# Kernel tuning notes

Measured on AMD Instinct MI355X. Metric: run time of the kernel, lower is better.

The kernel has to match this reference:

```python
import jax, jax.numpy as jnp
import numpy as np

B, N, IN_DIM = 8, 1024, 64
HID, OUT = 96, 128
NEG_SLOPE = 0.2
LN_EPS = 1e-5


def setup_inputs() -> dict:
    key = jax.random.key(0)
    ks = iter(jax.random.split(key, 32))
    d = {}
    d['x'] = jax.random.normal(next(ks), (B, N, IN_DIM), dtype=jnp.float32)
    d['adj'] = jax.random.randint(next(ks), (N, N), 0, 2, dtype=jnp.int32)
    # pre: LayerNorm + Linear(in->hid)
    d['ln_g'] = jnp.ones((IN_DIM,), jnp.float32)
    d['ln_b'] = jnp.zeros((IN_DIM,), jnp.float32)
    d['pre_w'] = jax.random.normal(next(ks), (IN_DIM, HID)) * 0.05
    d['pre_b'] = jnp.zeros((HID,), jnp.float32)
    # gat1: 3 heads of dim 32, concat; gat2-5: 1 head of dim 96, mean
    def gat_params(h, dim):
        w = jax.random.normal(next(ks), (HID, h * dim)) * 0.05
        a_s = jax.random.normal(next(ks), (h, dim)) * 0.05
        a_d = jax.random.normal(next(ks), (h, dim)) * 0.05
        return w, a_s, a_d
    d['g1_w'], d['g1_as'], d['g1_ad'] = gat_params(3, HID // 3)
    d['g2_w'], d['g2_as'], d['g2_ad'] = gat_params(1, HID)
    d['g3_w'], d['g3_as'], d['g3_ad'] = gat_params(1, HID)
    d['g4_w'], d['g4_as'], d['g4_ad'] = gat_params(1, HID)
    d['g5_w'], d['g5_as'], d['g5_ad'] = gat_params(1, HID)
    # sym_gate: Linear(2*hid -> hid//2), ELU, Linear(hid//2 -> 2), Sigmoid
    d['gate_w1'] = jax.random.normal(next(ks), (2 * HID, HID // 2)) * 0.05
    d['gate_b1'] = jnp.zeros((HID // 2,), jnp.float32)
    d['gate_w2'] = jax.random.normal(next(ks), (HID // 2, 2)) * 0.05
    d['gate_b2'] = jnp.zeros((2,), jnp.float32)
    # embed_proj: Linear(3*hid -> out)
    d['proj_w'] = jax.random.normal(next(ks), (3 * HID, OUT)) * 0.05
    d['proj_b'] = jnp.zeros((OUT,), jnp.float32)
    return d


def _gat(x, adj_mask, W, a_src, a_dst, concat):
    b, n, _ = x.shape
    h_heads, dim = a_src.shape
    h = (x @ W).reshape(b, n, h_heads, dim).transpose(0, 2, 1, 3)  # [B,H,N,D]
    e_src = jnp.einsum('bhnd,hd->bhn', h, a_src)
    e_dst = jnp.einsum('bhnd,hd->bhn', h, a_dst)
    # e[b,h,i,j] = leaky_relu(e_src[i] + e_dst[j])
    e = jax.nn.leaky_relu(e_src[..., :, None] + e_dst[..., None, :], NEG_SLOPE)
    e = jnp.where(adj_mask[None, None, :, :], e, jnp.float32(-1e9))
    attn = jax.nn.softmax(e, axis=-1)  # dropout is identity in eval mode
    out = jnp.einsum('bhij,bhjd->bhid', attn, h)
    if concat:
        return out.transpose(0, 2, 1, 3).reshape(b, n, h_heads * dim)
    return out.mean(axis=1)


def reference(x, adj, ln_g, ln_b, pre_w, pre_b,
              g1_w, g1_as, g1_ad, g2_w, g2_as, g2_ad,
              g3_w, g3_as, g3_ad, g4_w, g4_as, g4_ad,
              g5_w, g5_as, g5_ad,
              gate_w1, gate_b1, gate_w2, gate_b2, proj_w, proj_b):
    mask = adj > 0  # [N,N] bool
    # pre: LayerNorm -> Linear -> ELU (dropout = identity, eval mode)
    mu = x.mean(-1, keepdims=True)
    var = ((x - mu) ** 2).mean(-1, keepdims=True)
    xn = (x - mu) * jax.lax.rsqrt(var + LN_EPS) * ln_g + ln_b
    x0 = jax.nn.elu(xn @ pre_w + pre_b)
    x1 = jax.nn.elu(_gat(x0, mask, g1_w, g1_as, g1_ad, concat=True))
    x2 = jax.nn.elu(_gat(x1, mask, g2_w, g2_as, g2_ad, concat=False))
    pooled = jnp.concatenate([x1.mean(axis=1), x2.mean(axis=1)], axis=-1)  # [B,2*hid]
    gates = jax.nn.sigmoid(jax.nn.elu(pooled @ gate_w1 + gate_b1) @ gate_w2 + gate_b2)  # [B,2]
    w_t = gates[:, 0][:, None, None]
    w_r = gates[:, 1][:, None, None]
    td_in = (1.0 - w_t) * x1 + w_t * x2
    ra_in = (1.0 - w_r) * x1 + w_r * x2
    x4 = jax.nn.elu(_gat(td_in, mask, g4_w, g4_as, g4_ad, concat=False))
    x5 = jax.nn.elu(_gat(ra_in, mask, g5_w, g5_as, g5_ad, concat=False))
    stage_in = x2 + 0.5 * (w_t * x4 + w_r * x5)
    x3 = jax.nn.elu(_gat(stage_in, mask, g3_w, g3_as, g3_ad, concat=False))
    graph_token = jnp.concatenate([x3.mean(axis=1), x4.mean(axis=1), x5.mean(axis=1)], axis=-1)
    embed = jax.nn.elu(graph_token @ proj_w + proj_b)
    return (embed, gates[:, 0], gates[:, 1])
```

## Files before the change

### kernel.cpp

```cpp
#include <hip/hip_runtime.h>
#include <math.h>

#define Bq 8
#define Nn 1024
#define IND 64
#define HIDD 96

typedef __attribute__((ext_vector_type(8))) short bf16x8_t;
typedef __attribute__((ext_vector_type(4))) float f32x4_t;
typedef unsigned int u32;

__device__ __forceinline__ float elu_f(float x){ return x > 0.f ? x : __expf(x) - 1.f; }
__device__ __forceinline__ float lrelu_f(float x){ return x > 0.f ? x : 0.2f * x; }
__device__ __forceinline__ short f2bf(float f){
    union { float f; u32 u; } v; v.f = f;
    u32 r = (v.u + 0x7FFFu + ((v.u >> 16) & 1u)) >> 16;
    return (short)r;
}

__global__ __launch_bounds__(256) void pack_adj(const int* __restrict__ adj, u32* __restrict__ adjp)
{
    int w = blockIdx.x * 256 + threadIdx.x;
    int row = w >> 5, wc = w & 31;
    const int* p = adj + (size_t)row * Nn + wc * 32;
    u32 b = 0;
    #pragma unroll
    for (int e = 0; e < 32; e++) b |= (p[e] > 0 ? 1u : 0u) << e;
    adjp[w] = b;
}

struct PrepArgs { const float *W, *as_, *ad_; int H; };
struct Prep5 { PrepArgs a[5]; };

__global__ __launch_bounds__(96) void prep_w(Prep5 p, short* __restrict__ Wt)
{
    const int c = blockIdx.x, g = blockIdx.y, k = threadIdx.x;
    const PrepArgs A = p.a[g];
    float v = 0.f;
    if (c < 96) v = A.W[k * 96 + c];
    else {
        int q = c - 96, dim = 96 / A.H;
        if (q < A.H) { if (k >= q * dim && k < (q + 1) * dim) v = A.as_[k]; }
        else if (q < 2 * A.H) { int hh = q - A.H; if (k >= hh * dim && k < (hh + 1) * dim) v = A.ad_[k]; }
    }
    Wt[((size_t)g * 112 + c) * 96 + k] = f2bf(v);
}

__global__ __launch_bounds__(256) void pre_kernel(
    const float* __restrict__ x, const float* __restrict__ ln_g, const float* __restrict__ ln_b,
    const float* __restrict__ w, const float* __restrict__ bias, float* __restrict__ x0)
{
    __shared__ float xs[32][68];
    __shared__ float wl[IND * HIDD];
    __shared__ float gl[IND], bl[IND];
    __shared__ float mu[32], rv[32];
    const int t = threadIdx.x;
    const int i0 = blockIdx.x * 32, b = blockIdx.y;

    {
        const float4* w4 = (const float4*)w;
        float4* wl4 = (float4*)wl;
        #pragma unroll
        for (int m = 0; m < 6; m++) wl4[t + 256 * m] = w4[t + 256 * m];
    }
    if (t < IND) { gl[t] = ln_g[t]; bl[t] = ln_b[t]; }
    {
        const float4* xg = (const float4*)(x + ((size_t)b * Nn + i0) * IND);
        #pragma unroll
        for (int m = 0; m < 2; m++) {
            int idx = t + 256 * m;
            int r = idx >> 4, c4 = idx & 15;
            float4 v = xg[idx];
            xs[r][c4 * 4 + 0] = v.x; xs[r][c4 * 4 + 1] = v.y;
            xs[r][c4 * 4 + 2] = v.z; xs[r][c4 * 4 + 3] = v.w;
        }
    }
    __syncthreads();
    const int r = t >> 3, cg = t & 7;
    {
        float s = 0.f, s2 = 0.f;
        #pragma unroll
        for (int k = 0; k < 8; k++) { float v = xs[r][cg * 8 + k]; s += v; s2 += v * v; }
        #pragma unroll
        for (int m = 1; m < 8; m <<= 1) { s += __shfl_xor(s, m); s2 += __shfl_xor(s2, m); }
        if (cg == 0) {
            float mean = s * (1.f / IND);
            mu[r] = mean;
            rv[r] = rsqrtf(s2 * (1.f / IND) - mean * mean + 1e-5f);
        }
    }
    __syncthreads();
    float acc[12];
    #pragma unroll
    for (int c = 0; c < 12; c++) acc[c] = 0.f;
    const float mur = mu[r], rvr = rv[r];
    for (int k = 0; k < IND; k++) {
        float xn = (xs[r][k] - mur) * rvr * gl[k] + bl[k];
        const float4* wrow = (const float4*)(&wl[k * HIDD + cg * 12]);
        #pragma unroll
        for (int q = 0; q < 3; q++) {
            float4 wv = wrow[q];
            acc[q * 4 + 0] += xn * wv.x; acc[q * 4 + 1] += xn * wv.y;
            acc[q * 4 + 2] += xn * wv.z; acc[q * 4 + 3] += xn * wv.w;
        }
    }
    #pragma unroll
    for (int c = 0; c < 12; c++) acc[c] = elu_f(acc[c] + bias[cg * 12 + c]);
    float4* o4 = (float4*)(x0 + ((size_t)b * Nn + i0 + r) * HIDD + cg * 12);
    o4[0] = make_float4(acc[0], acc[1], acc[2], acc[3]);
    o4[1] = make_float4(acc[4], acc[5], acc[6], acc[7]);
    o4[2] = make_float4(acc[8], acc[9], acc[10], acc[11]);
}

struct HArgs {
    const float *xa, *xb, *xc;
    const short* Wt;
    float *es, *ed;
    short *ht;
    int mode, H;
};

__global__ __launch_bounds__(256) void h_mfma(HArgs a0, HArgs a1, const float* __restrict__ gates)
{
    const int t = threadIdx.x;
    const int lane = t & 63, w = t >> 6;
    const int node0 = blockIdx.x * 16;
    const int b = node0 >> 10, n0 = node0 & 1023;
    const HArgs A = blockIdx.y ? a1 : a0;
    const int row16 = lane & 15, grp = lane >> 4;

    float wt = 0.f, wr = 0.f;
    if (A.mode == 1) wt = gates[b * 2 + 0];
    else if (A.mode == 2) wt = gates[b * 2 + 1];
    else if (A.mode == 3) { wt = gates[b * 2 + 0]; wr = gates[b * 2 + 1]; }

    const size_t rowoff = (size_t)(node0 + row16) * HIDD;
    const int nt0 = (w < 3) ? 2 * w : 6;

    f32x4_t acc0 = {0.f,0.f,0.f,0.f}, acc1 = {0.f,0.f,0.f,0.f};
    #pragma unroll
    for (int ks = 0; ks < 3; ks++) {
        const int k0 = ks * 32 + grp * 8;
        float xv[8];
        {
            const float* pa = A.xa + rowoff + k0;
            float4 v0 = *(const float4*)pa, v1 = *(const float4*)(pa + 4);
            xv[0]=v0.x; xv[1]=v0.y; xv[2]=v0.z; xv[3]=v0.w;
            xv[4]=v1.x; xv[5]=v1.y; xv[6]=v1.z; xv[7]=v1.w;
        }
        if (A.mode == 1 || A.mode == 2) {
            const float* pb = A.xb + rowoff + k0;
            float4 u0 = *(const float4*)pb, u1 = *(const float4*)(pb + 4);
            float yv[8] = {u0.x,u0.y,u0.z,u0.w,u1.x,u1.y,u1.z,u1.w};
            #pragma unroll
            for (int e = 0; e < 8; e++) xv[e] = (1.f - wt) * xv[e] + wt * yv[e];
        } else if (A.mode == 3) {
            const float* pb = A.xb + rowoff + k0;
            const float* pc = A.xc + rowoff + k0;
            float4 u0 = *(const float4*)pb, u1 = *(const float4*)(pb + 4);
            float4 q0 = *(const float4*)pc, q1 = *(const float4*)(pc + 4);
            float yv[8] = {u0.x,u0.y,u0.z,u0.w,u1.x,u1.y,u1.z,u1.w};
            float zv[8] = {q0.x,q0.y,q0.z,q0.w,q1.x,q1.y,q1.z,q1.w};
            #pragma unroll
            for (int e = 0; e < 8; e++) xv[e] = xv[e] + 0.5f * (wt * yv[e] + wr * zv[e]);
        }
        bf16x8_t af;
        #pragma unroll
        for (int e = 0; e < 8; e++) af[e] = f2bf(xv[e]);

        {
            const short* wp0 = A.Wt + (size_t)(nt0 * 16 + row16) * 96 + k0;
            bf16x8_t bf0 = *(const bf16x8_t*)wp0;
            acc0 = __builtin_amdgcn_mfma_f32_16x16x32_bf16(af, bf0, acc0, 0, 0, 0);
        }
        if (w < 3) {
            const short* wp1 = A.Wt + (size_t)((nt0 + 1) * 16 + row16) * 96 + k0;
            bf16x8_t bf1 = *(const bf16x8_t*)wp1;
            acc1 = __builtin_amdgcn_mfma_f32_16x16x32_bf16(af, bf1, acc1, 0, 0, 0);
        }
    }
    if (w < 3) {
        u32 lo0 = ((u32)(unsigned short)f2bf(acc0[0])) | (((u32)(unsigned short)f2bf(acc0[1])) << 16);
        u32 hi0 = ((u32)(unsigned short)f2bf(acc0[2])) | (((u32)(unsigned short)f2bf(acc0[3])) << 16);
        int c0 = nt0 * 16 + row16;
        *(uint2*)(A.ht + ((size_t)b * 96 + c0) * Nn + n0 + grp * 4) = make_uint2(lo0, hi0);
        u32 lo1 = ((u32)(unsigned short)f2bf(acc1[0])) | (((u32)(unsigned short)f2bf(acc1[1])) << 16);
        u32 hi1 = ((u32)(unsigned short)f2bf(acc1[2])) | (((u32)(unsigned short)f2bf(acc1[3])) << 16);
        int c1 = c0 + 16;
        *(uint2*)(A.ht + ((size_t)b * 96 + c1) * Nn + n0 + grp * 4) = make_uint2(lo1, hi1);
    } else {
        int q = row16;
        if (q < 2 * A.H) {
            int head = (q < A.H) ? q : q - A.H;
            float* dst = ((q < A.H) ? A.es : A.ed) + ((size_t)b * A.H + head) * Nn + n0 + grp * 4;
            *(float4*)dst = make_float4(acc0[0], acc0[1], acc0[2], acc0[3]);
        }
    }
}

struct WArgs {
    const short* ht;
    const float* es;
    const float* ed;
    float* out;
    float* msum;
};

template<int DIM, int NH, bool DUAL>
__global__ __launch_bounds__(256) void ws_kernel(const u32* __restrict__ adjp, WArgs a0, WArgs a1)
{
    constexpr int NT = DIM / 16;
    __shared__ u32 adjl[16][33];
    __shared__ float esl[16];
    __shared__ float red[4][16][DIM + 1];
    __shared__ float redz[4][16];
    __shared__ float colsum[DIM];
    const int t = threadIdx.x;
    const int i0 = blockIdx.x * 16;
    const int by = blockIdx.y, b = blockIdx.z;
    const WArgs A = (DUAL && by) ? a1 : a0;
    const int h_in = DUAL ? 0 : by;
    const int colbase = h_in * DIM;

    if (t < 128) {
        int r = t >> 3, w4 = (t & 7) * 4;
        uint4 wv = *(const uint4*)(adjp + (size_t)(i0 + r) * 32 + w4);
        adjl[r][w4] = wv.x; adjl[r][w4 + 1] = wv.y; adjl[r][w4 + 2] = wv.z; adjl[r][w4 + 3] = wv.w;
    }
    if (t < 16) esl[t] = A.es[((size_t)b * NH + h_in) * Nn + i0 + t];
    if (t < DIM) colsum[t] = 0.f;
    __syncthreads();

    const int lane = t & 63, w = t >> 6;
    const int row16 = lane & 15, grp = lane >> 4;
    const int jb = w * 256;
    const float es_r = esl[row16];
    const float* edp = A.ed + ((size_t)b * NH + h_in) * Nn + jb + grp * 8;
    const short* hrow = A.ht + ((size_t)b * 96 + colbase + row16) * Nn + jb + grp * 8;

    f32x4_t acc[NT];
    #pragma unroll
    for (int n = 0; n < NT; n++) acc[n] = (f32x4_t){0.f, 0.f, 0.f, 0.f};
    f32x4_t accz = {0.f, 0.f, 0.f, 0.f};
    bf16x8_t ones;
    #pragma unroll
    for (int e = 0; e < 8; e++) ones[e] = (short)0x3F80;

    #pragma unroll
    for (int ks = 0; ks < 8; ks++) {
        u32 bits = adjl[row16][w * 8 + ks] >> (grp * 8);
        float4 e0 = *(const float4*)(edp + ks * 32);
        float4 e1 = *(const float4*)(edp + ks * 32 + 4);
        float ev[8] = {e0.x, e0.y, e0.z, e0.w, e1.x, e1.y, e1.z, e1.w};
        bf16x8_t af;
        #pragma unroll
        for (int e = 0; e < 8; e++) {
            float p = __expf(lrelu_f(es_r + ev[e]));
            af[e] = f2bf(((bits >> e) & 1) ? p : 0.f);
        }
        #pragma unroll
        for (int n = 0; n < NT; n++) {
            bf16x8_t bf = *(const bf16x8_t*)(hrow + n * 16 * Nn + ks * 32);
            acc[n] = __builtin_amdgcn_mfma_f32_16x16x32_bf16(af, bf, acc[n], 0, 0, 0);
        }
        accz = __builtin_amdgcn_mfma_f32_16x16x32_bf16(af, ones, accz, 0, 0, 0);
    }

    #pragma unroll
    for (int n = 0; n < NT; n++)
        #pragma unroll
        for (int reg = 0; reg < 4; reg++)
            red[w][grp * 4 + reg][n * 16 + row16] = acc[n][reg];
    if (row16 == 0) {
        #pragma unroll
        for (int reg = 0; reg < 4; reg++) redz[w][grp * 4 + reg] = accz[reg];
    }
    __syncthreads();

    #pragma unroll
    for (int q = 0; q < (16 * DIM) / 256; q++) {
        int idx = t + q * 256;
        int r = idx / DIM, c = idx % DIM;
        float s = red[0][r][c] + red[1][r][c] + red[2][r][c] + red[3][r][c];
        float z = redz[0][r] + redz[1][r] + redz[2][r] + redz[3][r];
        float o = elu_f(s / z);
        A.out[((size_t)b * Nn + i0 + r) * HIDD + colbase + c] = o;
        atomicAdd(&colsum[c], o);
    }
    __syncthreads();
    if (t < DIM) atomicAdd(&A.msum[b * HIDD + colbase + t], colsum[t]);
}

__global__ __launch_bounds__(64) void gates_kernel(
    const float* __restrict__ x1s, const float* __restrict__ x2s,
    const float* __restrict__ w1, const float* __restrict__ b1,
    const float* __restrict__ w2, const float* __restrict__ b2,
    float* __restrict__ gates, float* __restrict__ d_out)
{
    __shared__ float pl[192], hid[48];
    const int b = blockIdx.x, t = threadIdx.x;
    for (int k = t; k < 192; k += 64)
        pl[k] = ((k < HIDD) ? x1s[b * HIDD + k] : x2s[b * HIDD + k - HIDD]) * (1.f / Nn);
    __syncthreads();
    if (t < 48) {
        float acc = b1[t];
        for (int k = 0; k < 192; k++) acc += pl[k] * w1[k * 48 + t];
        hid[t] = elu_f(acc);
    }
    __syncthreads();
    if (t < 2) {
        float acc = b2[t];
        for (int k = 0; k < 48; k++) acc += hid[k] * w2[k * 2 + t];
        float g = 1.f / (1.f + __expf(-acc));
        gates[b * 2 + t] = g;
        d_out[1024 + t * 8 + b] = g;
    }
}

__global__ __launch_bounds__(128) void proj_kernel(
    const float* __restrict__ x3s, const float* __restrict__ x4s, const float* __restrict__ x5s,
    const float* __restrict__ w, const float* __restrict__ bias, float* __restrict__ d_out)
{
    __shared__ float tok[288];
    const int b = blockIdx.x, t = threadIdx.x;
    if (t < HIDD) {
        tok[t]            = x3s[b * HIDD + t] * (1.f / Nn);
        tok[HIDD + t]     = x4s[b * HIDD + t] * (1.f / Nn);
        tok[2 * HIDD + t] = x5s[b * HIDD + t] * (1.f / Nn);
    }
    __syncthreads();
    float acc = bias[t];
    for (int k = 0; k < 288; k++) acc += tok[k] * w[k * 128 + t];
    d_out[b * 128 + t] = elu_f(acc);
}

extern "C" void kernel_launch(void* const* d_in, const int* in_sizes, int n_in,
                              void* d_out, int out_size, void* d_ws, size_t ws_size,
                              hipStream_t stream)
{
    const float* x     = (const float*)d_in[0];
    const int*   adj   = (const int*)d_in[1];
    const float* ln_g  = (const float*)d_in[2];
    const float* ln_b  = (const float*)d_in[3];
    const float* pre_w = (const float*)d_in[4];
    const float* pre_b = (const float*)d_in[5];
    const float* g_w[5]  = {(const float*)d_in[6],  (const float*)d_in[9],  (const float*)d_in[12],
                            (const float*)d_in[15], (const float*)d_in[18]};
    const float* g_as[5] = {(const float*)d_in[7],  (const float*)d_in[10], (const float*)d_in[13],
                            (const float*)d_in[16], (const float*)d_in[19]};
    const float* g_ad[5] = {(const float*)d_in[8],  (const float*)d_in[11], (const float*)d_in[14],
                            (const float*)d_in[17], (const float*)d_in[20]};
    const float* gw1 = (const float*)d_in[21];
    const float* gb1 = (const float*)d_in[22];
    const float* gw2 = (const float*)d_in[23];
    const float* gb2 = (const float*)d_in[24];
    const float* pw  = (const float*)d_in[25];
    const float* pb  = (const float*)d_in[26];
    float* out = (float*)d_out;

    float* ws = (float*)d_ws;
    const size_t SZ = (size_t)Bq * Nn * HIDD;
    float* x0 = ws;
    float* x1 = ws + 1 * SZ;
    float* x2 = ws + 2 * SZ;
    float* x3 = ws + 3 * SZ;
    float* x4 = ws + 4 * SZ;
    float* x5 = ws + 5 * SZ;
    float* esb = ws + 6 * SZ;
    float* edb = esb + 24576;
    short* ht0 = (short*)(edb + 24576);
    short* ht1 = ht0 + (size_t)Bq * 96 * Nn;
    short* wtb = ht1 + (size_t)Bq * 96 * Nn;
    float* msb = (float*)(wtb + 5 * 112 * 96);
    float* ms1 = msb, *ms2 = msb + 768, *ms3 = msb + 1536, *ms4 = msb + 2304, *ms5 = msb + 3072;
    float* gts = msb + 3840;
    u32*   adjp = (u32*)(gts + 16);

    const dim3 blk256(256);

    hipMemsetAsync(msb, 0, 3840 * sizeof(float), stream);
    {
        Prep5 P;
        for (int g = 0; g < 5; g++) { P.a[g].W = g_w[g]; P.a[g].as_ = g_as[g]; P.a[g].ad_ = g_ad[g]; P.a[g].H = (g == 0) ? 3 : 1; }
        prep_w<<<dim3(112, 5), dim3(96), 0, stream>>>(P, wtb);
    }
    pack_adj<<<dim3(128), blk256, 0, stream>>>(adj, adjp);
    pre_kernel<<<dim3(Nn / 32, Bq), blk256, 0, stream>>>(x, ln_g, ln_b, pre_w, pre_b, x0);

    const dim3 hgrid1(Bq * Nn / 16, 1), hgrid2(Bq * Nn / 16, 2);

    {
        HArgs A; A.xa = x0; A.xb = nullptr; A.xc = nullptr;
        A.Wt = wtb + 0 * 112 * 96; A.es = esb; A.ed = edb; A.ht = ht0; A.mode = 0; A.H = 3;
        h_mfma<<<hgrid1, blk256, 0, stream>>>(A, A, gts);
        WArgs W0; W0.ht = ht0; W0.es = esb; W0.ed = edb; W0.out = x1; W0.msum = ms1;
        ws_kernel<32, 3, false><<<dim3(Nn / 16, 3, Bq), blk256, 0, stream>>>(adjp, W0, W0);
    }
    {
        HArgs A; A.xa = x1; A.xb = nullptr; A.xc = nullptr;
        A.Wt = wtb + 1 * 112 * 96; A.es = esb; A.ed = edb; A.ht = ht0; A.mode = 0; A.H = 1;
        h_mfma<<<hgrid1, blk256, 0, stream>>>(A, A, gts);
        WArgs W0; W0.ht = ht0; W0.es = esb; W0.ed = edb; W0.out = x2; W0.msum = ms2;
        ws_kernel<96, 1, false><<<dim3(Nn / 16, 1, Bq), blk256, 0, stream>>>(adjp, W0, W0);
    }
    gates_kernel<<<dim3(Bq), dim3(64), 0, stream>>>(ms1, ms2, gw1, gb1, gw2, gb2, gts, out);

    {
        HArgs A0; A0.xa = x1; A0.xb = x2; A0.xc = nullptr;
        A0.Wt = wtb + 3 * 112 * 96; A0.es = esb; A0.ed = edb; A0.ht = ht0; A0.mode = 1; A0.H = 1;
        HArgs A1; A1.xa = x1; A1.xb = x2; A1.xc = nullptr;
        A1.Wt = wtb + 4 * 112 * 96; A1.es = esb + 8192; A1.ed = edb + 8192; A1.ht = ht1; A1.mode = 2; A1.H = 1;
        h_mfma<<<hgrid2, blk256, 0, stream>>>(A0, A1, gts);
        WArgs W0; W0.ht = ht0; W0.es = esb; W0.ed = edb; W0.out = x4; W0.msum = ms4;
        WArgs W1; W1.ht = ht1; W1.es = esb + 8192; W1.ed = edb + 8192; W1.out = x5; W1.msum = ms5;
        ws_kernel<96, 1, true><<<dim3(Nn / 16, 2, Bq), blk256, 0, stream>>>(adjp, W0, W1);
    }
    {
        HArgs A; A.xa = x2; A.xb = x4; A.xc = x5;
        A.Wt = wtb + 2 * 112 * 96; A.es = esb; A.ed = edb; A.ht = ht0; A.mode = 3; A.H = 1;
        h_mfma<<<hgrid1, blk256, 0, stream>>>(A, A, gts);
        WArgs W0; W0.ht = ht0; W0.es = esb; W0.ed = edb; W0.out = x3; W0.msum = ms3;
        ws_kernel<96, 1, false><<<dim3(Nn / 16, 1, Bq), blk256, 0, stream>>>(adjp, W0, W0);
    }

    proj_kernel<<<dim3(Bq), dim3(128), 0, stream>>>(ms3, ms4, ms5, pw, pb, out);
}
```

Measured before the change: 260.2 us.

## Fuse projections into aggregation kernels using linearity of gated inputs

```diff
diff --git a/kernel.cpp b/kernel.cpp
--- a/kernel.cpp
+++ b/kernel.cpp
@@ -3,8 +3,6 @@
 
 #define Bq 8
 #define Nn 1024
-#define IND 64
-#define HIDD 96
 
 typedef __attribute__((ext_vector_type(8))) short bf16x8_t;
 typedef __attribute__((ext_vector_type(4))) float f32x4_t;
@@ -14,306 +12,333 @@
 __device__ __forceinline__ float lrelu_f(float x){ return x > 0.f ? x : 0.2f * x; }
 __device__ __forceinline__ short f2bf(float f){
     union { float f; u32 u; } v; v.f = f;
-    u32 r = (v.u + 0x7FFFu + ((v.u >> 16) & 1u)) >> 16;
-    return (short)r;
-}
-
-__global__ __launch_bounds__(256) void pack_adj(const int* __restrict__ adj, u32* __restrict__ adjp)
-{
-    int w = blockIdx.x * 256 + threadIdx.x;
-    int row = w >> 5, wc = w & 31;
-    const int* p = adj + (size_t)row * Nn + wc * 32;
-    u32 b = 0;
+    return (short)((v.u + 0x7FFFu + ((v.u >> 16) & 1u)) >> 16);
+}
+__device__ __forceinline__ u32 pk2(float a, float b){
+    return (u32)(unsigned short)f2bf(a) | ((u32)(unsigned short)f2bf(b) << 16);
+}
+__device__ __forceinline__ bf16x8_t cvt8(const float* p){
+    bf16x8_t r;
     #pragma unroll
-    for (int e = 0; e < 32; e++) b |= (p[e] > 0 ? 1u : 0u) << e;
-    adjp[w] = b;
-}
-
-struct PrepArgs { const float *W, *as_, *ad_; int H; };
-struct Prep5 { PrepArgs a[5]; };
-
-__global__ __launch_bounds__(96) void prep_w(Prep5 p, short* __restrict__ Wt)
-{
-    const int c = blockIdx.x, g = blockIdx.y, k = threadIdx.x;
-    const PrepArgs A = p.a[g];
-    float v = 0.f;
-    if (c < 96) v = A.W[k * 96 + c];
-    else {
-        int q = c - 96, dim = 96 / A.H;
-        if (q < A.H) { if (k >= q * dim && k < (q + 1) * dim) v = A.as_[k]; }
-        else if (q < 2 * A.H) { int hh = q - A.H; if (k >= hh * dim && k < (hh + 1) * dim) v = A.ad_[k]; }
-    }
-    Wt[((size_t)g * 112 + c) * 96 + k] = f2bf(v);
-}
-
-__global__ __launch_bounds__(256) void pre_kernel(
+    for (int e = 0; e < 8; e++) r[e] = f2bf(p[e]);
+    return r;
+}
+
+struct PrepP {
+    const float *W0,*W1,*W2,*W3,*W4;
+    const float *s0,*s1,*s2,*s3,*s4;
+    const float *d0,*d1,*d2,*d3,*d4;
+};
+
+__global__ __launch_bounds__(256) void setup_kernel(
+    PrepP P, const int* __restrict__ adj, const float* __restrict__ pre_w,
+    u32* __restrict__ adjp, short* __restrict__ wtb, short* __restrict__ wpre,
+    float* __restrict__ msz)
+{
+    const int bid = blockIdx.x, t = threadIdx.x;
+    if (bid < 128) {
+        int w = bid * 256 + t;
+        int row = w >> 5, wc = w & 31;
+        const int* p = adj + (size_t)row * Nn + wc * 32;
+        u32 bset = 0;
+        #pragma unroll
+        for (int e = 0; e < 32; e++) bset |= (p[e] > 0 ? 1u : 0u) << e;
+        adjp[w] = bset;
+    } else if (bid < 338) {
+        int idx = (bid - 128) * 256 + t;
+        int g = idx / 10752, rem = idx % 10752;
+        int c = rem / 96, k = rem % 96;
+        const float* W  = (g==0)?P.W0:(g==1)?P.W1:(g==2)?P.W2:(g==3)?P.W3:P.W4;
+        const float* as = (g==0)?P.s0:(g==1)?P.s1:(g==2)?P.s2:(g==3)?P.s3:P.s4;
+        const float* ad = (g==0)?P.d0:(g==1)?P.d1:(g==2)?P.d2:(g==3)?P.d3:P.d4;
+        const int H = (g == 0) ? 3 : 1, dim = 96 / H;
+        float v = 0.f;
+        if (c < 96) v = W[k * 96 + c];
+        else {
+            int q = c - 96;
+            if (q < H) {
+                int base = q * dim; float s = 0.f;
+                for (int d = 0; d < dim; d++) s += W[k * 96 + base + d] * as[base + d];
+                v = s;
+            } else if (q < 2 * H) {
+                int base = (q - H) * dim; float s = 0.f;
+                for (int d = 0; d < dim; d++) s += W[k * 96 + base + d] * ad[base + d];
+                v = s;
+            }
+        }
+        wtb[idx] = f2bf(v);
+    } else if (bid < 362) {
+        int idx = (bid - 338) * 256 + t;
+        int c = idx >> 6, k = idx & 63;
+        wpre[idx] = f2bf(pre_w[k * 96 + c]);
+    } else {
+        int idx = (bid - 362) * 256 + t;
+        if (idx < 3856) msz[idx] = 0.f;
+    }
+}
+
+__global__ __launch_bounds__(256) void pre_h1(
     const float* __restrict__ x, const float* __restrict__ ln_g, const float* __restrict__ ln_b,
-    const float* __restrict__ w, const float* __restrict__ bias, float* __restrict__ x0)
-{
-    __shared__ float xs[32][68];
-    __shared__ float wl[IND * HIDD];
-    __shared__ float gl[IND], bl[IND];
-    __shared__ float mu[32], rv[32];
+    const short* __restrict__ wpre, const float* __restrict__ pre_b,
+    const short* __restrict__ Wt1, short* __restrict__ ht1,
+    float* __restrict__ es1, float* __restrict__ ed1)
+{
+    __shared__ short xsA[16][72];
+    __shared__ float xs0[16][100];
     const int t = threadIdx.x;
-    const int i0 = blockIdx.x * 32, b = blockIdx.y;
-
-    {
-        const float4* w4 = (const float4*)w;
-        float4* wl4 = (float4*)wl;
-        #pragma unroll
-        for (int m = 0; m < 6; m++) wl4[t + 256 * m] = w4[t + 256 * m];
-    }
-    if (t < IND) { gl[t] = ln_g[t]; bl[t] = ln_b[t]; }
-    {
-        const float4* xg = (const float4*)(x + ((size_t)b * Nn + i0) * IND);
-        #pragma unroll
-        for (int m = 0; m < 2; m++) {
-            int idx = t + 256 * m;
-            int r = idx >> 4, c4 = idx & 15;
-            float4 v = xg[idx];
-            xs[r][c4 * 4 + 0] = v.x; xs[r][c4 * 4 + 1] = v.y;
-            xs[r][c4 * 4 + 2] = v.z; xs[r][c4 * 4 + 3] = v.w;
-        }
-    }
-    __syncthreads();
-    const int r = t >> 3, cg = t & 7;
-    {
-        float s = 0.f, s2 = 0.f;
-        #pragma unroll
-        for (int k = 0; k < 8; k++) { float v = xs[r][cg * 8 + k]; s += v; s2 += v * v; }
-        #pragma unroll
-        for (int m = 1; m < 8; m <<= 1) { s += __shfl_xor(s, m); s2 += __shfl_xor(s2, m); }
-        if (cg == 0) {
-            float mean = s * (1.f / IND);
-            mu[r] = mean;
-            rv[r] = rsqrtf(s2 * (1.f / IND) - mean * mean + 1e-5f);
-        }
-    }
-    __syncthreads();
-    float acc[12];
-    #pragma unroll
-    for (int c = 0; c < 12; c++) acc[c] = 0.f;
-    const float mur = mu[r], rvr = rv[r];
-    for (int k = 0; k < IND; k++) {
-        float xn = (xs[r][k] - mur) * rvr * gl[k] + bl[k];
-        const float4* wrow = (const float4*)(&wl[k * HIDD + cg * 12]);
-        #pragma unroll
-        for (int q = 0; q < 3; q++) {
-            float4 wv = wrow[q];
-            acc[q * 4 + 0] += xn * wv.x; acc[q * 4 + 1] += xn * wv.y;
-            acc[q * 4 + 2] += xn * wv.z; acc[q * 4 + 3] += xn * wv.w;
-        }
-    }
-    #pragma unroll
-    for (int c = 0; c < 12; c++) acc[c] = elu_f(acc[c] + bias[cg * 12 + c]);
-    float4* o4 = (float4*)(x0 + ((size_t)b * Nn + i0 + r) * HIDD + cg * 12);
-    o4[0] = make_float4(acc[0], acc[1], acc[2], acc[3]);
-    o4[1] = make_float4(acc[4], acc[5], acc[6], acc[7]);
-    o4[2] = make_float4(acc[8], acc[9], acc[10], acc[11]);
-}
-
-struct HArgs {
-    const float *xa, *xb, *xc;
-    const short* Wt;
-    float *es, *ed;
-    short *ht;
-    int mode, H;
+    const int bid = blockIdx.x;
+    const int b = bid >> 6, n0 = (bid & 63) * 16;
+    {
+        int r = t >> 4, c4 = t & 15;
+        float4 v = *(const float4*)(x + ((size_t)b * Nn + n0 + r) * 64 + c4 * 4);
+        float s = v.x + v.y + v.z + v.w;
+        float s2 = v.x*v.x + v.y*v.y + v.z*v.z + v.w*v.w;
+        #pragma unroll
+        for (int m = 1; m < 16; m <<= 1) { s += __shfl_xor(s, m); s2 += __shfl_xor(s2, m); }
+        float mu = s * (1.f / 64), rv = rsqrtf(s2 * (1.f / 64) - mu * mu + 1e-5f);
+        float4 g = *(const float4*)(ln_g + c4 * 4);
+        float4 bb = *(const float4*)(ln_b + c4 * 4);
+        float xn0 = (v.x - mu) * rv * g.x + bb.x;
+        float xn1 = (v.y - mu) * rv * g.y + bb.y;
+        float xn2 = (v.z - mu) * rv * g.z + bb.z;
+        float xn3 = (v.w - mu) * rv * g.w + bb.w;
+        *(uint2*)&xsA[r][c4 * 4] = make_uint2(pk2(xn0, xn1), pk2(xn2, xn3));
+    }
+    __syncthreads();
+    const int lane = t & 63, w = t >> 6;
+    const int row16 = lane & 15, grp = lane >> 4;
+    for (int tile = w; tile < 6; tile += 4) {
+        f32x4_t acc = {0.f,0.f,0.f,0.f};
+        #pragma unroll
+        for (int ks = 0; ks < 2; ks++) {
+            int k0 = ks * 32 + grp * 8;
+            bf16x8_t af = *(const bf16x8_t*)&xsA[row16][k0];
+            bf16x8_t bf = *(const bf16x8_t*)(wpre + (size_t)(tile * 16 + row16) * 64 + k0);
+            acc = __builtin_amdgcn_mfma_f32_16x16x32_bf16(af, bf, acc, 0, 0, 0);
+        }
+        int col = tile * 16 + row16;
+        float pbv = pre_b[col];
+        #pragma unroll
+        for (int reg = 0; reg < 4; reg++)
+            xs0[grp * 4 + reg][col] = elu_f(acc[reg] + pbv);
+    }
+    __syncthreads();
+    for (int tile = w; tile < 7; tile += 4) {
+        f32x4_t acc = {0.f,0.f,0.f,0.f};
+        #pragma unroll
+        for (int ks = 0; ks < 3; ks++) {
+            int k0 = ks * 32 + grp * 8;
+            bf16x8_t af = cvt8(&xs0[row16][k0]);
+            bf16x8_t bf = *(const bf16x8_t*)(Wt1 + (size_t)(tile * 16 + row16) * 96 + k0);
+            acc = __builtin_amdgcn_mfma_f32_16x16x32_bf16(af, bf, acc, 0, 0, 0);
+        }
+        int col = tile * 16 + row16;
+        if (tile < 6) {
+            *(uint2*)(ht1 + ((size_t)b * 96 + col) * Nn + n0 + grp * 4) =
+                make_uint2(pk2(acc[0], acc[1]), pk2(acc[2], acc[3]));
+        } else {
+            int q = row16;
+            if (q < 3)
+                *(float4*)(es1 + ((size_t)b * 3 + q) * Nn + n0 + grp * 4) =
+                    make_float4(acc[0], acc[1], acc[2], acc[3]);
+            else if (q < 6)
+                *(float4*)(ed1 + ((size_t)b * 3 + (q - 3)) * Nn + n0 + grp * 4) =
+                    make_float4(acc[0], acc[1], acc[2], acc[3]);
+        }
+    }
+}
+
+struct WSArgs {
+    const float *es, *ed;
+    const short *ht;
+    float *ms;
+    int nmat, mode0;
+    const short *W0, *W1, *W2;
+    float *T0, *T1, *T2;
+    short *oHt; float *oEs, *oEd;
 };
 
-__global__ __launch_bounds__(256) void h_mfma(HArgs a0, HArgs a1, const float* __restrict__ gates)
-{
+template<int NH>
+__global__ __launch_bounds__(256) void ws_fused(const u32* __restrict__ adjp, WSArgs a0, WSArgs a1)
+{
+    constexpr int DIMH = 96 / NH, NT = DIMH / 16;
+    __shared__ float xrows[16][100];
+    __shared__ float red[4][16][97];
+    __shared__ float redz[4][16];
+    __shared__ u32 adjl[16][33];
+    __shared__ float esl[NH * 16];
     const int t = threadIdx.x;
-    const int lane = t & 63, w = t >> 6;
-    const int node0 = blockIdx.x * 16;
-    const int b = node0 >> 10, n0 = node0 & 1023;
-    const HArgs A = blockIdx.y ? a1 : a0;
-    const int row16 = lane & 15, grp = lane >> 4;
-
-    float wt = 0.f, wr = 0.f;
-    if (A.mode == 1) wt = gates[b * 2 + 0];
-    else if (A.mode == 2) wt = gates[b * 2 + 1];
-    else if (A.mode == 3) { wt = gates[b * 2 + 0]; wr = gates[b * 2 + 1]; }
-
-    const size_t rowoff = (size_t)(node0 + row16) * HIDD;
-    const int nt0 = (w < 3) ? 2 * w : 6;
-
-    f32x4_t acc0 = {0.f,0.f,0.f,0.f}, acc1 = {0.f,0.f,0.f,0.f};
-    #pragma unroll
-    for (int ks = 0; ks < 3; ks++) {
-        const int k0 = ks * 32 + grp * 8;
-        float xv[8];
-        {
-            const float* pa = A.xa + rowoff + k0;
-            float4 v0 = *(const float4*)pa, v1 = *(const float4*)(pa + 4);
-            xv[0]=v0.x; xv[1]=v0.y; xv[2]=v0.z; xv[3]=v0.w;
-            xv[4]=v1.x; xv[5]=v1.y; xv[6]=v1.z; xv[7]=v1.w;
-        }
-        if (A.mode == 1 || A.mode == 2) {
-            const float* pb = A.xb + rowoff + k0;
-            float4 u0 = *(const float4*)pb, u1 = *(const float4*)(pb + 4);
-            float yv[8] = {u0.x,u0.y,u0.z,u0.w,u1.x,u1.y,u1.z,u1.w};
-            #pragma unroll
-            for (int e = 0; e < 8; e++) xv[e] = (1.f - wt) * xv[e] + wt * yv[e];
-        } else if (A.mode == 3) {
-            const float* pb = A.xb + rowoff + k0;
-            const float* pc = A.xc + rowoff + k0;
-            float4 u0 = *(const float4*)pb, u1 = *(const float4*)(pb + 4);
-            float4 q0 = *(const float4*)pc, q1 = *(const float4*)(pc + 4);
-            float yv[8] = {u0.x,u0.y,u0.z,u0.w,u1.x,u1.y,u1.z,u1.w};
-            float zv[8] = {q0.x,q0.y,q0.z,q0.w,q1.x,q1.y,q1.z,q1.w};
-            #pragma unroll
-            for (int e = 0; e < 8; e++) xv[e] = xv[e] + 0.5f * (wt * yv[e] + wr * zv[e]);
-        }
-        bf16x8_t af;
-        #pragma unroll
-        for (int e = 0; e < 8; e++) af[e] = f2bf(xv[e]);
-
-        {
-            const short* wp0 = A.Wt + (size_t)(nt0 * 16 + row16) * 96 + k0;
-            bf16x8_t bf0 = *(const bf16x8_t*)wp0;
-            acc0 = __builtin_amdgcn_mfma_f32_16x16x32_bf16(af, bf0, acc0, 0, 0, 0);
-        }
-        if (w < 3) {
-            const short* wp1 = A.Wt + (size_t)((nt0 + 1) * 16 + row16) * 96 + k0;
-            bf16x8_t bf1 = *(const bf16x8_t*)wp1;
-            acc1 = __builtin_amdgcn_mfma_f32_16x16x32_bf16(af, bf1, acc1, 0, 0, 0);
-        }
-    }
-    if (w < 3) {
-        u32 lo0 = ((u32)(unsigned short)f2bf(acc0[0])) | (((u32)(unsigned short)f2bf(acc0[1])) << 16);
-        u32 hi0 = ((u32)(unsigned short)f2bf(acc0[2])) | (((u32)(unsigned short)f2bf(acc0[3])) << 16);
-        int c0 = nt0 * 16 + row16;
-        *(uint2*)(A.ht + ((size_t)b * 96 + c0) * Nn + n0 + grp * 4) = make_uint2(lo0, hi0);
-        u32 lo1 = ((u32)(unsigned short)f2bf(acc1[0])) | (((u32)(unsigned short)f2bf(acc1[1])) << 16);
-        u32 hi1 = ((u32)(unsigned short)f2bf(acc1[2])) | (((u32)(unsigned short)f2bf(acc1[3])) << 16);
-        int c1 = c0 + 16;
-        *(uint2*)(A.ht + ((size_t)b * 96 + c1) * Nn + n0 + grp * 4) = make_uint2(lo1, hi1);
-    } else {
-        int q = row16;
-        if (q < 2 * A.H) {
-            int head = (q < A.H) ? q : q - A.H;
-            float* dst = ((q < A.H) ? A.es : A.ed) + ((size_t)b * A.H + head) * Nn + n0 + grp * 4;
-            *(float4*)dst = make_float4(acc0[0], acc0[1], acc0[2], acc0[3]);
-        }
-    }
-}
-
-struct WArgs {
-    const short* ht;
-    const float* es;
-    const float* ed;
-    float* out;
-    float* msum;
-};
-
-template<int DIM, int NH, bool DUAL>
-__global__ __launch_bounds__(256) void ws_kernel(const u32* __restrict__ adjp, WArgs a0, WArgs a1)
-{
-    constexpr int NT = DIM / 16;
-    __shared__ u32 adjl[16][33];
-    __shared__ float esl[16];
-    __shared__ float red[4][16][DIM + 1];
-    __shared__ float redz[4][16];
-    __shared__ float colsum[DIM];
-    const int t = threadIdx.x;
-    const int i0 = blockIdx.x * 16;
-    const int by = blockIdx.y, b = blockIdx.z;
-    const WArgs A = (DUAL && by) ? a1 : a0;
-    const int h_in = DUAL ? 0 : by;
-    const int colbase = h_in * DIM;
+    const int i0 = blockIdx.x * 16, b = blockIdx.z;
+    const WSArgs A = blockIdx.y ? a1 : a0;
 
     if (t < 128) {
         int r = t >> 3, w4 = (t & 7) * 4;
         uint4 wv = *(const uint4*)(adjp + (size_t)(i0 + r) * 32 + w4);
-        adjl[r][w4] = wv.x; adjl[r][w4 + 1] = wv.y; adjl[r][w4 + 2] = wv.z; adjl[r][w4 + 3] = wv.w;
-    }
-    if (t < 16) esl[t] = A.es[((size_t)b * NH + h_in) * Nn + i0 + t];
-    if (t < DIM) colsum[t] = 0.f;
+        adjl[r][w4] = wv.x; adjl[r][w4+1] = wv.y; adjl[r][w4+2] = wv.z; adjl[r][w4+3] = wv.w;
+    }
+    if (t < NH * 16)
+        esl[t] = A.es[((size_t)b * NH + (t >> 4)) * Nn + i0 + (t & 15)];
     __syncthreads();
 
     const int lane = t & 63, w = t >> 6;
     const int row16 = lane & 15, grp = lane >> 4;
     const int jb = w * 256;
-    const float es_r = esl[row16];
-    const float* edp = A.ed + ((size_t)b * NH + h_in) * Nn + jb + grp * 8;
-    const short* hrow = A.ht + ((size_t)b * 96 + colbase + row16) * Nn + jb + grp * 8;
-
-    f32x4_t acc[NT];
-    #pragma unroll
-    for (int n = 0; n < NT; n++) acc[n] = (f32x4_t){0.f, 0.f, 0.f, 0.f};
-    f32x4_t accz = {0.f, 0.f, 0.f, 0.f};
     bf16x8_t ones;
     #pragma unroll
     for (int e = 0; e < 8; e++) ones[e] = (short)0x3F80;
 
     #pragma unroll
-    for (int ks = 0; ks < 8; ks++) {
-        u32 bits = adjl[row16][w * 8 + ks] >> (grp * 8);
-        float4 e0 = *(const float4*)(edp + ks * 32);
-        float4 e1 = *(const float4*)(edp + ks * 32 + 4);
-        float ev[8] = {e0.x, e0.y, e0.z, e0.w, e1.x, e1.y, e1.z, e1.w};
-        bf16x8_t af;
-        #pragma unroll
-        for (int e = 0; e < 8; e++) {
-            float p = __expf(lrelu_f(es_r + ev[e]));
-            af[e] = f2bf(((bits >> e) & 1) ? p : 0.f);
+    for (int h = 0; h < NH; h++) {
+        const float es_r = esl[h * 16 + row16];
+        const float* edp = A.ed + ((size_t)b * NH + h) * Nn + jb + grp * 8;
+        const short* hb_ = A.ht + ((size_t)b * 96 + h * DIMH) * Nn + jb + grp * 8;
+        f32x4_t acc[NT];
+        f32x4_t accz = {0.f,0.f,0.f,0.f};
+        #pragma unroll
+        for (int n = 0; n < NT; n++) acc[n] = (f32x4_t){0.f,0.f,0.f,0.f};
+        #pragma unroll
+        for (int ks = 0; ks < 8; ks++) {
+            u32 bits = adjl[row16][w * 8 + ks] >> (grp * 8);
+            float4 e0 = *(const float4*)(edp + ks * 32);
+            float4 e1 = *(const float4*)(edp + ks * 32 + 4);
+            float ev[8] = {e0.x,e0.y,e0.z,e0.w,e1.x,e1.y,e1.z,e1.w};
+            bf16x8_t af;
+            #pragma unroll
+            for (int e = 0; e < 8; e++) {
+                float p = __expf(lrelu_f(es_r + ev[e]));
+                af[e] = f2bf(((bits >> e) & 1) ? p : 0.f);
+            }
+            #pragma unroll
+            for (int n = 0; n < NT; n++) {
+                bf16x8_t bf = *(const bf16x8_t*)(hb_ + (size_t)(n * 16 + row16) * Nn + ks * 32);
+                acc[n] = __builtin_amdgcn_mfma_f32_16x16x32_bf16(af, bf, acc[n], 0, 0, 0);
+            }
+            accz = __builtin_amdgcn_mfma_f32_16x16x32_bf16(af, ones, accz, 0, 0, 0);
         }
         #pragma unroll
         for (int n = 0; n < NT; n++) {
-            bf16x8_t bf = *(const bf16x8_t*)(hrow + n * 16 * Nn + ks * 32);
-            acc[n] = __builtin_amdgcn_mfma_f32_16x16x32_bf16(af, bf, acc[n], 0, 0, 0);
-        }
-        accz = __builtin_amdgcn_mfma_f32_16x16x32_bf16(af, ones, accz, 0, 0, 0);
-    }
-
-    #pragma unroll
-    for (int n = 0; n < NT; n++)
-        #pragma unroll
-        for (int reg = 0; reg < 4; reg++)
-            red[w][grp * 4 + reg][n * 16 + row16] = acc[n][reg];
-    if (row16 == 0) {
-        #pragma unroll
-        for (int reg = 0; reg < 4; reg++) redz[w][grp * 4 + reg] = accz[reg];
-    }
-    __syncthreads();
-
-    #pragma unroll
-    for (int q = 0; q < (16 * DIM) / 256; q++) {
-        int idx = t + q * 256;
-        int r = idx / DIM, c = idx % DIM;
-        float s = red[0][r][c] + red[1][r][c] + red[2][r][c] + red[3][r][c];
-        float z = redz[0][r] + redz[1][r] + redz[2][r] + redz[3][r];
-        float o = elu_f(s / z);
-        A.out[((size_t)b * Nn + i0 + r) * HIDD + colbase + c] = o;
-        atomicAdd(&colsum[c], o);
-    }
-    __syncthreads();
-    if (t < DIM) atomicAdd(&A.msum[b * HIDD + colbase + t], colsum[t]);
-}
-
-__global__ __launch_bounds__(64) void gates_kernel(
-    const float* __restrict__ x1s, const float* __restrict__ x2s,
-    const float* __restrict__ w1, const float* __restrict__ b1,
-    const float* __restrict__ w2, const float* __restrict__ b2,
-    float* __restrict__ gates, float* __restrict__ d_out)
-{
-    __shared__ float pl[192], hid[48];
-    const int b = blockIdx.x, t = threadIdx.x;
-    for (int k = t; k < 192; k += 64)
-        pl[k] = ((k < HIDD) ? x1s[b * HIDD + k] : x2s[b * HIDD + k - HIDD]) * (1.f / Nn);
+            #pragma unroll
+            for (int reg = 0; reg < 4; reg++)
+                red[w][grp * 4 + reg][n * 16 + row16] = acc[n][reg];
+        }
+        if (row16 == 0) {
+            #pragma unroll
+            for (int reg = 0; reg < 4; reg++) redz[w][grp * 4 + reg] = accz[reg];
+        }
+        __syncthreads();
+        #pragma unroll
+        for (int idx = t; idx < 16 * DIMH; idx += 256) {
+            int r = idx / DIMH, c = idx % DIMH;
+            float s = red[0][r][c] + red[1][r][c] + red[2][r][c] + red[3][r][c];
+            float z = redz[0][r] + redz[1][r] + redz[2][r] + redz[3][r];
+            xrows[r][h * DIMH + c] = elu_f(s / z);
+        }
+        __syncthreads();
+    }
+
+    if (t < 96) {
+        float s = 0.f;
+        #pragma unroll
+        for (int r = 0; r < 16; r++) s += xrows[r][t];
+        atomicAdd(A.ms + b * 96 + t, s);
+    }
+
+    for (int job = w; job < A.nmat * 7; job += 4) {
+        int mat = job / 7, tile = job - mat * 7;
+        const short* Wm = (mat == 0) ? A.W0 : (mat == 1) ? A.W1 : A.W2;
+        f32x4_t acc = {0.f,0.f,0.f,0.f};
+        #pragma unroll
+        for (int ks = 0; ks < 3; ks++) {
+            int k0 = ks * 32 + grp * 8;
+            bf16x8_t af = cvt8(&xrows[row16][k0]);
+            bf16x8_t bf = *(const bf16x8_t*)(Wm + (size_t)(tile * 16 + row16) * 96 + k0);
+            acc = __builtin_amdgcn_mfma_f32_16x16x32_bf16(af, bf, acc, 0, 0, 0);
+        }
+        int col = tile * 16 + row16;
+        if (mat == 0 && A.mode0 == 2) {
+            if (tile < 6) {
+                *(uint2*)(A.oHt + ((size_t)b * 96 + col) * Nn + i0 + grp * 4) =
+                    make_uint2(pk2(acc[0], acc[1]), pk2(acc[2], acc[3]));
+            } else if (row16 == 0) {
+                *(float4*)(A.oEs + (size_t)b * Nn + i0 + grp * 4) = make_float4(acc[0],acc[1],acc[2],acc[3]);
+            } else if (row16 == 1) {
+                *(float4*)(A.oEd + (size_t)b * Nn + i0 + grp * 4) = make_float4(acc[0],acc[1],acc[2],acc[3]);
+            }
+        } else {
+            float* Td = (mat == 0) ? A.T0 : (mat == 1) ? A.T1 : A.T2;
+            *(float4*)(Td + ((size_t)b * 112 + col) * Nn + i0 + grp * 4) =
+                make_float4(acc[0], acc[1], acc[2], acc[3]);
+        }
+    }
+}
+
+__global__ __launch_bounds__(256) void gates_combine(
+    const float* __restrict__ ms1, const float* __restrict__ ms2,
+    const float* __restrict__ gw1, const float* __restrict__ gb1,
+    const float* __restrict__ gw2, const float* __restrict__ gb2,
+    const float* __restrict__ U4, const float* __restrict__ V4,
+    const float* __restrict__ U5, const float* __restrict__ V5,
+    short* __restrict__ ht4, float* __restrict__ es4, float* __restrict__ ed4,
+    short* __restrict__ ht5, float* __restrict__ es5, float* __restrict__ ed5,
+    float* __restrict__ gts, float* __restrict__ d_out)
+{
+    __shared__ float pl[192], hid[48], gsh[2];
+    const int t = threadIdx.x, b = blockIdx.z, y = blockIdx.y, rr = blockIdx.x;
+    if (t < 192) pl[t] = ((t < 96) ? ms1[b * 96 + t] : ms2[b * 96 + t - 96]) * (1.f / Nn);
     __syncthreads();
     if (t < 48) {
-        float acc = b1[t];
-        for (int k = 0; k < 192; k++) acc += pl[k] * w1[k * 48 + t];
-        hid[t] = elu_f(acc);
+        float a = gb1[t];
+        for (int k = 0; k < 192; k++) a += pl[k] * gw1[k * 48 + t];
+        hid[t] = elu_f(a);
     }
     __syncthreads();
     if (t < 2) {
-        float acc = b2[t];
-        for (int k = 0; k < 48; k++) acc += hid[k] * w2[k * 2 + t];
-        float g = 1.f / (1.f + __expf(-acc));
-        gates[b * 2 + t] = g;
-        d_out[1024 + t * 8 + b] = g;
+        float a = gb2[t];
+        for (int k = 0; k < 48; k++) a += hid[k] * gw2[k * 2 + t];
+        float g = 1.f / (1.f + __expf(-a));
+        gsh[t] = g;
+        if (rr == 0 && y == 0) { gts[b * 2 + t] = g; d_out[1024 + t * 8 + b] = g; }
+    }
+    __syncthreads();
+    const float wg = gsh[y];
+    size_t off = ((size_t)b * 112 + rr) * Nn + t * 4;
+    float4 u = *(const float4*)((y ? U5 : U4) + off);
+    float4 v = *(const float4*)((y ? V5 : V4) + off);
+    float o0 = (1.f - wg) * u.x + wg * v.x;
+    float o1 = (1.f - wg) * u.y + wg * v.y;
+    float o2 = (1.f - wg) * u.z + wg * v.z;
+    float o3 = (1.f - wg) * u.w + wg * v.w;
+    if (rr < 96) {
+        short* Hh = (y ? ht5 : ht4) + ((size_t)b * 96 + rr) * Nn + t * 4;
+        *(uint2*)Hh = make_uint2(pk2(o0, o1), pk2(o2, o3));
+    } else if (rr == 96) {
+        *(float4*)((y ? es5 : es4) + (size_t)b * Nn + t * 4) = make_float4(o0, o1, o2, o3);
+    } else {
+        *(float4*)((y ? ed5 : ed4) + (size_t)b * Nn + t * 4) = make_float4(o0, o1, o2, o3);
+    }
+}
+
+__global__ __launch_bounds__(256) void combine3(
+    const float* __restrict__ gts, const float* __restrict__ U3,
+    const float* __restrict__ V34, const float* __restrict__ V35,
+    short* __restrict__ ht3, float* __restrict__ es3, float* __restrict__ ed3)
+{
+    const int t = threadIdx.x, b = blockIdx.z, rr = blockIdx.x;
+    const float wt = gts[b * 2], wr = gts[b * 2 + 1];
+    size_t off = ((size_t)b * 112 + rr) * Nn + t * 4;
+    float4 u = *(const float4*)(U3 + off);
+    float4 p = *(const float4*)(V34 + off);
+    float4 q = *(const float4*)(V35 + off);
+    float o0 = u.x + 0.5f * (wt * p.x + wr * q.x);
+    float o1 = u.y + 0.5f * (wt * p.y + wr * q.y);
+    float o2 = u.z + 0.5f * (wt * p.z + wr * q.z);
+    float o3 = u.w + 0.5f * (wt * p.w + wr * q.w);
+    if (rr < 96) {
+        *(uint2*)(ht3 + ((size_t)b * 96 + rr) * Nn + t * 4) = make_uint2(pk2(o0, o1), pk2(o2, o3));
+    } else if (rr == 96) {
+        *(float4*)(es3 + (size_t)b * Nn + t * 4) = make_float4(o0, o1, o2, o3);
+    } else {
+        *(float4*)(ed3 + (size_t)b * Nn + t * 4) = make_float4(o0, o1, o2, o3);
     }
 }
 
@@ -323,10 +348,10 @@
 {
     __shared__ float tok[288];
     const int b = blockIdx.x, t = threadIdx.x;
-    if (t < HIDD) {
-        tok[t]            = x3s[b * HIDD + t] * (1.f / Nn);
-        tok[HIDD + t]     = x4s[b * HIDD + t] * (1.f / Nn);
-        tok[2 * HIDD + t] = x5s[b * HIDD + t] * (1.f / Nn);
+    if (t < 96) {
+        tok[t]       = x3s[b * 96 + t] * (1.f / Nn);
+        tok[96 + t]  = x4s[b * 96 + t] * (1.f / Nn);
+        tok[192 + t] = x5s[b * 96 + t] * (1.f / Nn);
     }
     __syncthreads();
     float acc = bias[t];
@@ -358,70 +383,81 @@
     const float* pb  = (const float*)d_in[26];
     float* out = (float*)d_out;
 
-    float* ws = (float*)d_ws;
-    const size_t SZ = (size_t)Bq * Nn * HIDD;
-    float* x0 = ws;
-    float* x1 = ws + 1 * SZ;
-    float* x2 = ws + 2 * SZ;
-    float* x3 = ws + 3 * SZ;
-    float* x4 = ws + 4 * SZ;
-    float* x5 = ws + 5 * SZ;
-    float* esb = ws + 6 * SZ;
-    float* edb = esb + 24576;
-    short* ht0 = (short*)(edb + 24576);
-    short* ht1 = ht0 + (size_t)Bq * 96 * Nn;
-    short* wtb = ht1 + (size_t)Bq * 96 * Nn;
-    float* msb = (float*)(wtb + 5 * 112 * 96);
+    float* F = (float*)d_ws;
+    const size_t SZT = (size_t)Bq * 112 * Nn;
+    float* msb = F;
     float* ms1 = msb, *ms2 = msb + 768, *ms3 = msb + 1536, *ms4 = msb + 2304, *ms5 = msb + 3072;
     float* gts = msb + 3840;
-    u32*   adjp = (u32*)(gts + 16);
-
-    const dim3 blk256(256);
-
-    hipMemsetAsync(msb, 0, 3840 * sizeof(float), stream);
-    {
-        Prep5 P;
-        for (int g = 0; g < 5; g++) { P.a[g].W = g_w[g]; P.a[g].as_ = g_as[g]; P.a[g].ad_ = g_ad[g]; P.a[g].H = (g == 0) ? 3 : 1; }
-        prep_w<<<dim3(112, 5), dim3(96), 0, stream>>>(P, wtb);
-    }
-    pack_adj<<<dim3(128), blk256, 0, stream>>>(adj, adjp);
-    pre_kernel<<<dim3(Nn / 32, Bq), blk256, 0, stream>>>(x, ln_g, ln_b, pre_w, pre_b, x0);
-
-    const dim3 hgrid1(Bq * Nn / 16, 1), hgrid2(Bq * Nn / 16, 2);
-
-    {
-        HArgs A; A.xa = x0; A.xb = nullptr; A.xc = nullptr;
-        A.Wt = wtb + 0 * 112 * 96; A.es = esb; A.ed = edb; A.ht = ht0; A.mode = 0; A.H = 3;
-        h_mfma<<<hgrid1, blk256, 0, stream>>>(A, A, gts);
-        WArgs W0; W0.ht = ht0; W0.es = esb; W0.ed = edb; W0.out = x1; W0.msum = ms1;
-        ws_kernel<32, 3, false><<<dim3(Nn / 16, 3, Bq), blk256, 0, stream>>>(adjp, W0, W0);
-    }
-    {
-        HArgs A; A.xa = x1; A.xb = nullptr; A.xc = nullptr;
-        A.Wt = wtb + 1 * 112 * 96; A.es = esb; A.ed = edb; A.ht = ht0; A.mode = 0; A.H = 1;
-        h_mfma<<<hgrid1, blk256, 0, stream>>>(A, A, gts);
-        WArgs W0; W0.ht = ht0; W0.es = esb; W0.ed = edb; W0.out = x2; W0.msum = ms2;
-        ws_kernel<96, 1, false><<<dim3(Nn / 16, 1, Bq), blk256, 0, stream>>>(adjp, W0, W0);
-    }
-    gates_kernel<<<dim3(Bq), dim3(64), 0, stream>>>(ms1, ms2, gw1, gb1, gw2, gb2, gts, out);
-
-    {
-        HArgs A0; A0.xa = x1; A0.xb = x2; A0.xc = nullptr;
-        A0.Wt = wtb + 3 * 112 * 96; A0.es = esb; A0.ed = edb; A0.ht = ht0; A0.mode = 1; A0.H = 1;
-        HArgs A1; A1.xa = x1; A1.xb = x2; A1.xc = nullptr;
-        A1.Wt = wtb + 4 * 112 * 96; A1.es = esb + 8192; A1.ed = edb + 8192; A1.ht = ht1; A1.mode = 2; A1.H = 1;
-        h_mfma<<<hgrid2, blk256, 0, stream>>>(A0, A1, gts);
-        WArgs W0; W0.ht = ht0; W0.es = esb; W0.ed = edb; W0.out = x4; W0.msum = ms4;
-        WArgs W1; W1.ht = ht1; W1.es = esb + 8192; W1.ed = edb + 8192; W1.out = x5; W1.msum = ms5;
-        ws_kernel<96, 1, true><<<dim3(Nn / 16, 2, Bq), blk256, 0, stream>>>(adjp, W0, W1);
-    }
-    {
-        HArgs A; A.xa = x2; A.xb = x4; A.xc = x5;
-        A.Wt = wtb + 2 * 112 * 96; A.es = esb; A.ed = edb; A.ht = ht0; A.mode = 3; A.H = 1;
-        h_mfma<<<hgrid1, blk256, 0, stream>>>(A, A, gts);
-        WArgs W0; W0.ht = ht0; W0.es = esb; W0.ed = edb; W0.out = x3; W0.msum = ms3;
-        ws_kernel<96, 1, false><<<dim3(Nn / 16, 1, Bq), blk256, 0, stream>>>(adjp, W0, W0);
-    }
-
+    float* es1 = msb + 3856;
+    float* ed1 = es1 + 24576;
+    float* es2 = ed1 + 24576; float* ed2 = es2 + 8192;
+    float* es3 = ed2 + 8192;  float* ed3 = es3 + 8192;
+    float* es4 = ed3 + 8192;  float* ed4 = es4 + 8192;
+    float* es5 = ed4 + 8192;  float* ed5 = es5 + 8192;
+    float* U4  = ed5 + 8192;
+    float* U5  = U4 + SZT;
+    float* V4  = U5 + SZT;
+    float* V5  = V4 + SZT;
+    float* U3  = V5 + SZT;
+    float* V34 = U3 + SZT;
+    float* V35 = V34 + SZT;
+    u32*  adjp = (u32*)(V35 + SZT);
+    short* wtb = (short*)(adjp + 32768);
+    short* wpre = wtb + 5 * 10752;
+    short* ht1 = wpre + 6144;
+    short* ht2 = ht1 + (size_t)Bq * 96 * Nn;
+    short* ht3 = ht2 + (size_t)Bq * 96 * Nn;
+    short* ht4 = ht3 + (size_t)Bq * 96 * Nn;
+    short* ht5 = ht4 + (size_t)Bq * 96 * Nn;
+
+    const dim3 blk(256);
+
+    {
+        PrepP P;
+        P.W0 = g_w[0]; P.W1 = g_w[1]; P.W2 = g_w[2]; P.W3 = g_w[3]; P.W4 = g_w[4];
+        P.s0 = g_as[0]; P.s1 = g_as[1]; P.s2 = g_as[2]; P.s3 = g_as[3]; P.s4 = g_as[4];
+        P.d0 = g_ad[0]; P.d1 = g_ad[1]; P.d2 = g_ad[2]; P.d3 = g_ad[3]; P.d4 = g_ad[4];
+        setup_kernel<<<dim3(378), blk, 0, stream>>>(P, adj, pre_w, adjp, wtb, wpre, msb);
+    }
+
+    pre_h1<<<dim3(512), blk, 0, stream>>>(x, ln_g, ln_b, wpre, pre_b, wtb, ht1, es1, ed1);
+
+    {
+        WSArgs B; B.es = es1; B.ed = ed1; B.ht = ht1; B.ms = ms1;
+        B.nmat = 3; B.mode0 = 2;
+        B.W0 = wtb + 1 * 10752; B.W1 = wtb + 3 * 10752; B.W2 = wtb + 4 * 10752;
+        B.T0 = nullptr; B.T1 = U4; B.T2 = U5;
+        B.oHt = ht2; B.oEs = es2; B.oEd = ed2;
+        ws_fused<3><<<dim3(64, 1, Bq), blk, 0, stream>>>(adjp, B, B);
+    }
+    {
+        WSArgs C; C.es = es2; C.ed = ed2; C.ht = ht2; C.ms = ms2;
+        C.nmat = 3; C.mode0 = 1;
+        C.W0 = wtb + 3 * 10752; C.W1 = wtb + 4 * 10752; C.W2 = wtb + 2 * 10752;
+        C.T0 = V4; C.T1 = V5; C.T2 = U3;
+        C.oHt = nullptr; C.oEs = nullptr; C.oEd = nullptr;
+        ws_fused<1><<<dim3(64, 1, Bq), blk, 0, stream>>>(adjp, C, C);
+    }
+    gates_combine<<<dim3(98, 2, Bq), blk, 0, stream>>>(ms1, ms2, gw1, gb1, gw2, gb2,
+                                                       U4, V4, U5, V5,
+                                                       ht4, es4, ed4, ht5, es5, ed5, gts, out);
+    {
+        WSArgs E0; E0.es = es4; E0.ed = ed4; E0.ht = ht4; E0.ms = ms4;
+        E0.nmat = 1; E0.mode0 = 1; E0.W0 = wtb + 2 * 10752; E0.W1 = nullptr; E0.W2 = nullptr;
+        E0.T0 = V34; E0.T1 = nullptr; E0.T2 = nullptr;
+        E0.oHt = nullptr; E0.oEs = nullptr; E0.oEd = nullptr;
+        WSArgs E1 = E0;
+        E1.es = es5; E1.ed = ed5; E1.ht = ht5; E1.ms = ms5; E1.T0 = V35;
+        ws_fused<1><<<dim3(64, 2, Bq), blk, 0, stream>>>(adjp, E0, E1);
+    }
+    combine3<<<dim3(98, 1, Bq), blk, 0, stream>>>(gts, U3, V34, V35, ht3, es3, ed3);
+    {
+        WSArgs G; G.es = es3; G.ed = ed3; G.ht = ht3; G.ms = ms3;
+        G.nmat = 0; G.mode0 = 1;
+        G.W0 = nullptr; G.W1 = nullptr; G.W2 = nullptr;
+        G.T0 = nullptr; G.T1 = nullptr; G.T2 = nullptr;
+        G.oHt = nullptr; G.oEs = nullptr; G.oEd = nullptr;
+        ws_fused<1><<<dim3(64, 1, Bq), blk, 0, stream>>>(adjp, G, G);
+    }
     proj_kernel<<<dim3(Bq), dim3(128), 0, stream>>>(ms3, ms4, ms5, pw, pb, out);
 }
```

Measured after the change: 242.6 us. -6.8%, faster.
